# Optimization experiments

Measured on AMD Instinct MI355X. Metric: run time of the kernel, lower is better.

Reference implementation:

```python
import jax, jax.numpy as jnp
import numpy as np

B, N, H, L, K = 8, 2048, 256, 4, 16
G, M0, M1, C = 512, 256, 128, 128
EPS = 1e-5


def _rn(k, shape, scale):
    return jax.random.normal(k, shape, jnp.float32) * jnp.float32(scale)


def setup_inputs() -> dict:
    key = jax.random.key(0)
    ks = jax.random.split(key, 16)
    z, o = jnp.zeros, jnp.ones
    return {
        "x": jax.random.normal(ks[0], (B, N, 3), jnp.float32),
        "batch": jnp.repeat(jnp.arange(B, dtype=jnp.int32)[:, None], N, axis=1),
        "Wf": _rn(ks[1], (3, H), 0.5), "bf": z(H),
        "Wnn": _rn(ks[2], (H, H), H ** -0.5), "bnn": z(H),
        "g1": o((L, H)), "b1": z((L, H)),
        "We": _rn(ks[3], (L, 2 * H, H), (2 * H) ** -0.5), "be": z((L, H)),
        "g2": o((L, H)), "b2": z((L, H)),
        "Wl": _rn(ks[4], (L, H, H), H ** -0.5), "bl": z((L, H)),
        "alpha": _rn(ks[5], (L,), 0.1),
        "gg": o(H), "bgb": z(H),
        "Wg": _rn(ks[6], (H, G), H ** -0.5), "bg2": z(G),
        "Wm1": _rn(ks[7], (G, M0), G ** -0.5), "bm1": z(M0),
        "Wm2": _rn(ks[8], (M0, M1), M0 ** -0.5), "bm2": z(M1),
        "Wm3": _rn(ks[9], (M1, C), M1 ** -0.5), "bm3": z(C),
    }


def _bn(x, g, b):
    # BatchNorm1d training-mode math over all nodes (axes B,N), per channel
    m = x.mean(axis=(0, 1))
    v = x.var(axis=(0, 1))
    return (x - m) * jax.lax.rsqrt(v + EPS) * g + b


def _dgcnn(x, We, be):
    # dynamic kNN graph in feature space, per cloud; x: [B,N,H]
    sq = jnp.sum(x * x, axis=-1)                                  # [B,N]
    d = sq[:, :, None] + sq[:, None, :] - 2.0 * jnp.einsum('bnd,bmd->bnm', x, x)
    idx = jax.lax.top_k(-d, K)[1]                                 # [B,N,K] (includes self)
    x_j = jax.vmap(lambda xb, ib: xb[ib])(x, idx)                 # [B,N,K,H]
    x_i = x[:, :, None, :]
    e = jnp.concatenate([jnp.broadcast_to(x_i, x_j.shape), x_j - x_i], axis=-1)
    msg = jnp.einsum('bnkf,fh->bnkh', e, We) + be                 # edge MLP
    return jnp.max(msg, axis=2)                                   # max aggregate


def _forward(x, Wf, bf, Wnn, bnn, g1, b1, We, be, g2, b2, Wl, bl, alpha,
             gg, bgb, Wg, bg2, Wm1, bm1, Wm2, bm2, Wm3, bm3):
    h = x @ Wf + bf                                               # ffm_x (Linear, scale=None)
    for i in range(L):
        t = h @ Wnn + bnn if i == 0 else h                        # nn_x only on first layer
        t = jax.nn.relu(_bn(t, g1[i], b1[i]))
        t = _dgcnn(t, We[i], be[i])
        t = jax.nn.relu(_bn(t, g2[i], b2[i]))
        t = t @ Wl[i] + bl[i]
        h = h + alpha[i] * t                                      # ResidualCoefficient
    t = jax.nn.relu(_bn(h, gg, bgb)) @ Wg + bg2
    p = jnp.max(t, axis=1)                                        # global max pool -> [B,G]
    p = jax.nn.relu(p @ Wm1 + bm1)
    p = jax.nn.relu(p @ Wm2 + bm2)
    return p @ Wm3 + bm3                                          # [B, n_components]


def reference(x, batch, Wf, bf, Wnn, bnn, g1, b1, We, be, g2, b2, Wl, bl, alpha,
              gg, bgb, Wg, bg2, Wm1, bm1, Wm2, bm2, Wm3, bm3):
    # batch ids are implied by the dense [B,N] layout; kept for signature fidelity
    del batch
    return _forward(x, Wf, bf, Wnn, bnn, g1, b1, We, be, g2, b2, Wl, bl, alpha,
                    gg, bgb, Wg, bg2, Wm1, bm1, Wm2, bm2, Wm3, bm3)
```

## Files before the change

### kernel.cpp

```cpp
#include <hip/hip_runtime.h>
#include <cfloat>

#define B_  8
#define N_  2048
#define H_  256
#define L_  4
#define K_  16
#define G_  512
#define M0_ 256
#define M1_ 128
#define C_  128
#define BN_ 16384
#define KP_ 768

typedef unsigned short ushort_t;
typedef __attribute__((ext_vector_type(8))) short short8;
typedef __attribute__((ext_vector_type(4))) float f32x4;

#define OFF_H     ((size_t)0)
#define OFF_APACK ((size_t)16777216)
#define OFF_SQ    ((size_t)67108864)
#define OFF_IDX   ((size_t)67174400)
#define OFF_STATS ((size_t)68222976)
#define OFF_SCSH  ((size_t)68227072)
#define OFF_BCAT  ((size_t)68229120)
#define OFF_P0    ((size_t)68231168)
#define OFF_P1    ((size_t)68247552)
#define OFF_P2    ((size_t)68255744)
#define OFF_D     ((size_t)69206016)
#define OFF_T     (OFF_D + (size_t)0)
#define OFF_UV    (OFF_D + (size_t)50331648)
#define OFF_QW    (OFF_D + (size_t)83886080)
#define OFF_PMAX  (OFF_D + (size_t)84672512)
#define WS_NEEDED ((size_t)203423744)

static __device__ __forceinline__ ushort_t f2bf(float f) {
    unsigned u = __float_as_uint(f);
    unsigned r = (u + 0x7fffu + ((u >> 16) & 1u)) >> 16;
    return (ushort_t)r;
}
static __device__ __forceinline__ float bf2f(ushort_t h) {
    return __uint_as_float(((unsigned)h) << 16);
}
static __device__ __forceinline__ void pack3(float v, ushort_t* A, size_t base, int f) {
    ushort_t hi = f2bf(v);
    ushort_t lo = f2bf(v - bf2f(hi));
    A[base + f] = hi; A[base + H_ + f] = lo; A[base + 2 * H_ + f] = hi;
}


__global__ void feat_pack(const float* __restrict__ x, const float* __restrict__ Wf,
                          const float* __restrict__ bfv, float* __restrict__ h,
                          ushort_t* __restrict__ Ap) {
    int pt = blockIdx.x;
    int f  = threadIdx.x;
    float x0 = x[pt * 3 + 0], x1 = x[pt * 3 + 1], x2 = x[pt * 3 + 2];
    float v = x0 * Wf[f] + x1 * Wf[H_ + f] + x2 * Wf[2 * H_ + f] + bfv[f];
    h[(size_t)pt * H_ + f] = v;
    pack3(v, Ap, (size_t)pt * KP_, f);
}

__global__ void pack_wT(const float* __restrict__ W, ushort_t* __restrict__ Qp, int Nd) {
    int n = blockIdx.x, k = threadIdx.x;
    float w = W[(size_t)k * Nd + n];
    ushort_t hi = f2bf(w), lo = f2bf(w - bf2f(hi));
    size_t base = (size_t)n * KP_;
    Qp[base + k] = hi; Qp[base + H_ + k] = hi; Qp[base + 2 * H_ + k] = lo;
}

__global__ void pack_qcat(const float* __restrict__ We_l, const float* __restrict__ be_l,
                          ushort_t* __restrict__ Qp, float* __restrict__ bcat) {
    int n = blockIdx.x, k = threadIdx.x;
    float w;
    if (n < H_) w = We_l[(size_t)k * H_ + n] - We_l[(size_t)H_ * H_ + (size_t)k * H_ + n];
    else        w = We_l[(size_t)H_ * H_ + (size_t)k * H_ + (n - H_)];
    ushort_t hi = f2bf(w), lo = f2bf(w - bf2f(hi));
    size_t base = (size_t)n * KP_;
    Qp[base + k] = hi; Qp[base + H_ + k] = hi; Qp[base + 2 * H_ + k] = lo;
    if (k == 0) bcat[n] = (n < H_) ? be_l[n] : 0.f;
}

__global__ __launch_bounds__(256) void mfma_gemm(
    const ushort_t* __restrict__ P, const ushort_t* __restrict__ Q,
    const float* __restrict__ aux, float* __restrict__ out,
    int Kd, int ldOut, int mode, const float* __restrict__ resid,
    const float* __restrict__ alphap, int aidx, double* __restrict__ stats,
    int nx) {
    __shared__ __align__(16) ushort_t As[128 * 32];
    __shared__ __align__(16) ushort_t Bs[128 * 32];
    __shared__ float cs1[4][64], cs2[4][64];
    int i0, j0;
    if (nx) {
        int blk = blockIdx.x;
        int z = blk & 7;
        int rest = blk >> 3;
        int xb = rest % nx;
        int ys = rest / nx;
        i0 = (z * 16 + ys) * 128;
        j0 = xb * 128;
    } else {
        i0 = blockIdx.y * 128; j0 = blockIdx.x * 128;
    }
    int tid = threadIdx.x;
    int lane = tid & 63, wave = tid >> 6;
    int wm = wave & 1, wn = wave >> 1;
    int m16 = lane & 15, kq = (lane >> 4) * 8;

    f32x4 acc[4][4];
    f32x4 zero = {0.f, 0.f, 0.f, 0.f};
#pragma unroll
    for (int i = 0; i < 4; ++i)
#pragma unroll
        for (int j = 0; j < 4; ++j) acc[i][j] = zero;

    int srow = tid >> 2;
    int skc  = (tid & 3) * 8;

    for (int k0 = 0; k0 < Kd; k0 += 32) {
#pragma unroll
        for (int s = 0; s < 2; ++s) {
            int row = srow + s * 64;
            const ushort_t* gpA = P + (size_t)(i0 + row) * Kd + k0 + skc;
            const ushort_t* gpB = Q + (size_t)(j0 + row) * Kd + k0 + skc;
            __builtin_amdgcn_global_load_lds(
                (const __attribute__((address_space(1))) void*)gpA,
                (__attribute__((address_space(3))) void*)(As + (size_t)(wave * 64 + s * 256) * 8),
                16, 0, 0);
            __builtin_amdgcn_global_load_lds(
                (const __attribute__((address_space(1))) void*)gpB,
                (__attribute__((address_space(3))) void*)(Bs + (size_t)(wave * 64 + s * 256) * 8),
                16, 0, 0);
        }
        __syncthreads();
        short8 af[4], bfr[4];
#pragma unroll
        for (int fi = 0; fi < 4; ++fi)
            af[fi] = *(const short8*)(As + (wm * 64 + fi * 16 + m16) * 32 + kq);
#pragma unroll
        for (int fj = 0; fj < 4; ++fj)
            bfr[fj] = *(const short8*)(Bs + (wn * 64 + fj * 16 + m16) * 32 + kq);
#pragma unroll
        for (int fi = 0; fi < 4; ++fi)
#pragma unroll
            for (int fj = 0; fj < 4; ++fj)
                acc[fi][fj] = __builtin_amdgcn_mfma_f32_16x16x32_bf16(
                    af[fi], bfr[fj], acc[fi][fj], 0, 0, 0);
        __syncthreads();
    }
    float alpha = (mode == 2) ? alphap[aidx] : 0.f;
    int rbase = i0 + wm * 64 + (lane >> 4) * 4;
    int cbase = j0 + wn * 64 + m16;
    float s1[4] = {0.f, 0.f, 0.f, 0.f}, s2[4] = {0.f, 0.f, 0.f, 0.f};
#pragma unroll
    for (int fi = 0; fi < 4; ++fi) {
#pragma unroll
        for (int fj = 0; fj < 4; ++fj) {
            int c = cbase + fj * 16;
            float a = aux[c];
#pragma unroll
            for (int r = 0; r < 4; ++r) {
                int gr = rbase + fi * 16 + r;
                size_t oidx = (size_t)gr * ldOut + c;
                float val;
                if (mode == 2) val = resid[oidx] + alpha * (acc[fi][fj][r] + a);
                else           val = acc[fi][fj][r] + a;
                out[oidx] = val;
                s1[fj] += val; s2[fj] += val * val;
            }
        }
    }
    if (stats) {
#pragma unroll
        for (int fj = 0; fj < 4; ++fj) {
            float a1 = s1[fj], a2 = s2[fj];
            a1 += __shfl_xor(a1, 16); a1 += __shfl_xor(a1, 32);
            a2 += __shfl_xor(a2, 16); a2 += __shfl_xor(a2, 32);
            if ((lane >> 4) == 0) {
                cs1[wave][fj * 16 + m16] = a1;
                cs2[wave][fj * 16 + m16] = a2;
            }
        }
        __syncthreads();
        if (tid < 128) {
            int wnl = tid >> 6, cl = tid & 63;
            float t1 = cs1[2 * wnl][cl] + cs1[2 * wnl + 1][cl];
            float t2 = cs2[2 * wnl][cl] + cs2[2 * wnl + 1][cl];
            int c = j0 + tid;
            atomicAdd(&stats[c], (double)t1);
            atomicAdd(&stats[H_ + c], (double)t2);
        }
    }
}

__global__ __launch_bounds__(256) void gram_sym(const ushort_t* __restrict__ Ap,
                                                const float* __restrict__ sqb,
                                                float* __restrict__ D) {
    __shared__ __align__(16) ushort_t As[128 * 32];
    __shared__ __align__(16) ushort_t Bs[128 * 32];
    __shared__ __align__(16) float stg[4][1280];
    int blk = blockIdx.x;
    int z = blk & 7;
    int p = blk >> 3;
    int bi = 0, rem = p;
    while (rem >= 16 - bi) { rem -= 16 - bi; ++bi; }
    int bj = bi + rem;
    const ushort_t* Pz = Ap + (size_t)z * N_ * KP_;
    const float* sqz = sqb + (size_t)z * N_;
    float* Dz = D + (size_t)z * N_ * N_;
    int i0 = bi * 128, j0 = bj * 128;

    int tid = threadIdx.x;
    int lane = tid & 63, wave = tid >> 6;
    int wm = wave & 1, wn = wave >> 1;
    int m16 = lane & 15, q4 = lane >> 4;
    int kq = q4 * 8;

    f32x4 acc[4][4];
    f32x4 zero = {0.f, 0.f, 0.f, 0.f};
#pragma unroll
    for (int i = 0; i < 4; ++i)
#pragma unroll
        for (int j = 0; j < 4; ++j) acc[i][j] = zero;

    int srow = tid >> 2;
    int skc  = (tid & 3) * 8;

    for (int k0 = 0; k0 < KP_; k0 += 32) {
        int kb = (k0 < 256) ? k0 : ((k0 < 512) ? k0 + 256 : k0 - 256);
#pragma unroll
        for (int s = 0; s < 2; ++s) {
            int row = srow + s * 64;
            const ushort_t* gpA = Pz + (size_t)(i0 + row) * KP_ + k0 + skc;
            const ushort_t* gpB = Pz + (size_t)(j0 + row) * KP_ + kb + skc;
            __builtin_amdgcn_global_load_lds(
                (const __attribute__((address_space(1))) void*)gpA,
                (__attribute__((address_space(3))) void*)(As + (size_t)(wave * 64 + s * 256) * 8),
                16, 0, 0);
            __builtin_amdgcn_global_load_lds(
                (const __attribute__((address_space(1))) void*)gpB,
                (__attribute__((address_space(3))) void*)(Bs + (size_t)(wave * 64 + s * 256) * 8),
                16, 0, 0);
        }
        __syncthreads();
        short8 af[4], bfr[4];
#pragma unroll
        for (int fi = 0; fi < 4; ++fi)
            af[fi] = *(const short8*)(As + (wm * 64 + fi * 16 + m16) * 32 + kq);
#pragma unroll
        for (int fj = 0; fj < 4; ++fj)
            bfr[fj] = *(const short8*)(Bs + (wn * 64 + fj * 16 + m16) * 32 + kq);
#pragma unroll
        for (int fi = 0; fi < 4; ++fi)
#pragma unroll
            for (int fj = 0; fj < 4; ++fj)
                acc[fi][fj] = __builtin_amdgcn_mfma_f32_16x16x32_bf16(
                    af[fi], bfr[fj], acc[fi][fj], 0, 0, 0);
        __syncthreads();
    }

    float* sg = stg[wave];
    float scl[4];
#pragma unroll
    for (int fj = 0; fj < 4; ++fj) scl[fj] = sqz[j0 + wn * 64 + fj * 16 + m16];
    float sr[4][4];
#pragma unroll
    for (int fi = 0; fi < 4; ++fi) {
        float4 s4 = *(const float4*)(sqz + i0 + wm * 64 + fi * 16 + q4 * 4);
        sr[fi][0] = s4.x; sr[fi][1] = s4.y; sr[fi][2] = s4.z; sr[fi][3] = s4.w;
    }

    int rr = lane >> 2, cc = lane & 3;
#pragma unroll
    for (int fi = 0; fi < 4; ++fi) {
#pragma unroll
        for (int fj = 0; fj < 4; ++fj)
#pragma unroll
            for (int r = 0; r < 4; ++r)
                sg[(q4 * 4 + r) * 68 + fj * 16 + m16] = scl[fj] - 2.f * acc[fi][fj][r];
        float* drow = Dz + (size_t)(i0 + wm * 64 + fi * 16 + rr) * N_ + j0 + wn * 64;
#pragma unroll
        for (int t = 0; t < 4; ++t) {
            int chunk = cc + 4 * t;
            f32x4 o = *(const f32x4*)(sg + rr * 68 + chunk * 4);
            __builtin_nontemporal_store(o, (f32x4*)(drow + chunk * 4));
        }
    }

    if (bi != bj) {
#pragma unroll
        for (int fi = 0; fi < 4; ++fi) {
#pragma unroll
            for (int fj = 0; fj < 4; ++fj)
#pragma unroll
                for (int r = 0; r < 4; ++r)
                    sg[(fj * 16 + m16) * 20 + q4 * 4 + r] =
                        sr[fi][r] - 2.f * acc[fi][fj][r];
            int chunk = lane & 3;
#pragma unroll
            for (int u = 0; u < 4; ++u) {
                int cr = (lane >> 2) + 16 * u;
                f32x4 o = *(const f32x4*)(sg + cr * 20 + chunk * 4);
                __builtin_nontemporal_store(o,
                    (f32x4*)(Dz + (size_t)(j0 + wn * 64 + cr) * N_ +
                             i0 + wm * 64 + fi * 16 + chunk * 4));
            }
        }
    }
}

__global__ __launch_bounds__(256) void topk16(const float* __restrict__ D,
                                              int* __restrict__ idxb) {
    __shared__ unsigned long long cand[4][256];
    __shared__ int cnt[4];
    int w = threadIdx.x >> 6, lane = threadIdx.x & 63;
    int row = blockIdx.x * 4 + w;
    const float* dp = D + (size_t)row * N_;
    unsigned sk[32];
#pragma unroll
    for (int t = 0; t < 8; ++t) {
        f32x4 v4 = __builtin_nontemporal_load((const f32x4*)(dp + t * 256 + lane * 4));
#pragma unroll
        for (int j = 0; j < 4; ++j) {
            unsigned u = __float_as_uint(v4[j]);
            sk[t * 4 + j] = (u & 0x80000000u) ? ~u : (u | 0x80000000u);
        }
    }
    if (lane == 0) cnt[w] = 0;
    unsigned vm = sk[0];
#pragma unroll
    for (int i = 1; i < 32; ++i) vm = min(vm, sk[i]);
#pragma unroll
    for (int k = 2; k <= 64; k <<= 1) {
#pragma unroll
        for (int j = k >> 1; j > 0; j >>= 1) {
            unsigned pv = __shfl_xor(vm, j);
            bool up = ((lane & k) == 0);
            bool lower = ((lane & j) == 0);
            unsigned mn = min(vm, pv), mx = max(vm, pv);
            vm = (lower == up) ? mn : mx;
        }
    }
    unsigned T = __shfl(vm, 15);
    __syncthreads();
#pragma unroll
    for (int i = 0; i < 32; ++i) {
        if (sk[i] <= T) {
            unsigned col = (unsigned)((i >> 2) * 256 + lane * 4 + (i & 3));
            int s = atomicAdd(&cnt[w], 1);
            if (s < 256) cand[w][s] = ((unsigned long long)sk[i] << 32) | col;
        }
    }
    __syncthreads();
    int cn = cnt[w];
    if (cn <= 64) {
        unsigned long long mykey = (lane < cn) ? cand[w][lane] : ~0ull;
        for (int it = 0; it < 16; ++it) {
            unsigned long long best = mykey;
#pragma unroll
            for (int off = 32; off; off >>= 1) {
                unsigned long long o = __shfl_xor(best, off);
                if (o < best) best = o;
            }
            if (mykey == best) mykey = ~0ull;
            if (lane == 0) idxb[row * 16 + it] = (int)(unsigned)(best & 0xffffffffu);
        }
    } else if (cn <= 256) {
        for (int it = 0; it < 16; ++it) {
            unsigned long long best = ~0ull;
            for (int i = lane; i < cn; i += 64) {
                unsigned long long c = cand[w][i];
                if (c < best) best = c;
            }
#pragma unroll
            for (int off = 32; off; off >>= 1) {
                unsigned long long o = __shfl_xor(best, off);
                if (o < best) best = o;
            }
            for (int i = lane; i < cn; i += 64)
                if (cand[w][i] == best) cand[w][i] = ~0ull;
            if (lane == 0) idxb[row * 16 + it] = (int)(unsigned)(best & 0xffffffffu);
        }
    } else {
        unsigned mask = 0;
        for (int it = 0; it < 16; ++it) {
            unsigned long long key = ~0ull;
#pragma unroll
            for (int i = 0; i < 32; ++i) {
                if (!((mask >> i) & 1u)) {
                    unsigned long long k2 = ((unsigned long long)sk[i] << 32) |
                        (unsigned)((i >> 2) * 256 + lane * 4 + (i & 3));
                    if (k2 < key) key = k2;
                }
            }
#pragma unroll
            for (int off = 32; off; off >>= 1) {
                unsigned long long o = __shfl_xor(key, off);
                if (o < key) key = o;
            }
            unsigned jc = (unsigned)(key & 0xffffffffu);
            int li = ((jc & 255) >> 2);
            int ii = ((jc >> 8) << 2) | (jc & 3);
            if (lane == li) mask |= 1u << ii;
            if (lane == 0) idxb[row * 16 + it] = (int)jc;
        }
    }
}

__global__ void gather_max(const float* __restrict__ uv, const int* __restrict__ idxb,
                           float* __restrict__ outp, double* __restrict__ stats) {
    int blk = blockIdx.x;
    int b = blk & 7;
    int strip = blk >> 3;
    int r0 = b * N_ + strip * 32;
    int f = threadIdx.x;
    float s1 = 0.f, s2 = 0.f;
    for (int rr = 0; rr < 32; ++rr) {
        int row = r0 + rr;
        const int* ip = idxb + row * 16;
        float m = -FLT_MAX;
#pragma unroll
        for (int k = 0; k < 16; ++k) {
            int j = ip[k];
            m = fmaxf(m, uv[((size_t)((b << 11) + j)) * 512 + 256 + f]);
        }
        float v = uv[(size_t)row * 512 + f] + m;
        outp[(size_t)row * H_ + f] = v;
        s1 += v; s2 += v * v;
    }
    atomicAdd(&stats[f], (double)s1);
    atomicAdd(&stats[H_ + f], (double)s2);
}

__global__ void bn_zero(double* s) { s[threadIdx.x] = 0.0; }

__global__ void bn_final(double* __restrict__ sums, const float* __restrict__ g,
                         const float* __restrict__ b, float* __restrict__ scsh) {
    int f = threadIdx.x;
    double m  = sums[f] / (double)BN_;
    double var = sums[H_ + f] / (double)BN_ - m * m;
    double inv = 1.0 / sqrt(var + 1e-5);
    float sc = g[f] * (float)inv;
    scsh[f] = sc;
    scsh[H_ + f] = b[f] - (float)m * sc;
    sums[f] = 0.0; sums[H_ + f] = 0.0;
}

__global__ void bn_apply_pack(const float* __restrict__ X, const float* __restrict__ scsh,
                              ushort_t* __restrict__ Ap, float* __restrict__ sq) {
    int tid = threadIdx.x;
    int row = blockIdx.x * 8 + (tid >> 5);
    int f0  = (tid & 31) * 8;
    const float* xp = X + (size_t)row * H_ + f0;
    f32x4 x0 = *(const f32x4*)(xp);
    f32x4 x1 = *(const f32x4*)(xp + 4);
    f32x4 sc0 = *(const f32x4*)(scsh + f0);
    f32x4 sc1 = *(const f32x4*)(scsh + f0 + 4);
    f32x4 sh0 = *(const f32x4*)(scsh + H_ + f0);
    f32x4 sh1 = *(const f32x4*)(scsh + H_ + f0 + 4);
    float v[8];
#pragma unroll
    for (int i = 0; i < 4; ++i) {
        v[i]     = fmaxf(x0[i] * sc0[i] + sh0[i], 0.f);
        v[i + 4] = fmaxf(x1[i] * sc1[i] + sh1[i], 0.f);
    }
    short8 hi8, lo8;
#pragma unroll
    for (int i = 0; i < 8; ++i) {
        ushort_t hi = f2bf(v[i]);
        ushort_t lo = f2bf(v[i] - bf2f(hi));
        hi8[i] = (short)hi; lo8[i] = (short)lo;
    }
    ushort_t* ap = Ap + (size_t)row * KP_ + f0;
    *(short8*)(ap)            = hi8;
    *(short8*)(ap + H_)       = lo8;
    *(short8*)(ap + 2 * H_)   = hi8;
    if (sq) {
        float s = 0.f;
#pragma unroll
        for (int i = 0; i < 8; ++i) s += v[i] * v[i];
#pragma unroll
        for (int off = 16; off; off >>= 1) s += __shfl_down(s, off, 32);
        if ((tid & 31) == 0) sq[row] = s;
    }
}

__global__ void maxpool1(const float* __restrict__ y, float* __restrict__ pmax) {
    int b = blockIdx.x, gc = blockIdx.y, nc = blockIdx.z;
    int g = gc * 256 + threadIdx.x;
    const float* yb = y + ((size_t)b * N_ + (size_t)nc * 128) * G_;
    float m = -FLT_MAX;
    for (int n = 0; n < 128; ++n) m = fmaxf(m, yb[(size_t)n * G_ + g]);
    pmax[((size_t)(b * 16 + nc)) * G_ + g] = m;
}

__global__ void maxpool2(const float* __restrict__ pmax, float* __restrict__ p) {
    int b = blockIdx.x;
    int g = blockIdx.y * 256 + threadIdx.x;
    float m = -FLT_MAX;
    for (int c = 0; c < 16; ++c) m = fmaxf(m, pmax[((size_t)(b * 16 + c)) * G_ + g]);
    p[(size_t)b * G_ + g] = m;
}

__global__ __launch_bounds__(256) void head_gemm(const float* __restrict__ A,
                                                 const float* __restrict__ W,
                                                 const float* __restrict__ bias,
                                                 float* __restrict__ Cc,
                                                 int Kd, int Nd, int relu) {
    int m = blockIdx.x;
    int c0 = blockIdx.y * 64;
    int cl = threadIdx.x & 63;
    int ks = threadIdx.x >> 6;
    int kper = Kd >> 2;
    const float* Ap = A + (size_t)m * Kd + (size_t)ks * kper;
    const float* Wp = W + (size_t)ks * kper * Nd + c0 + cl;
    float acc = 0.f;
    for (int k = 0; k < kper; k += 8) {
#pragma unroll
        for (int u2 = 0; u2 < 8; ++u2)
            acc += Ap[k + u2] * Wp[(size_t)(k + u2) * Nd];
    }
    __shared__ float red[4][64];
    red[ks][cl] = acc;
    __syncthreads();
    if (ks == 0) {
        float s = red[0][cl] + red[1][cl] + red[2][cl] + red[3][cl] + bias[c0 + cl];
        if (relu) s = fmaxf(s, 0.f);
        Cc[(size_t)m * Nd + c0 + cl] = s;
    }
}

extern "C" void kernel_launch(void* const* d_in, const int* in_sizes, int n_in,
                              void* d_out, int out_size, void* d_ws, size_t ws_size,
                              hipStream_t stream) {
    (void)in_sizes; (void)n_in; (void)out_size;
    if (ws_size < WS_NEEDED) return;

    const float* x    = (const float*)d_in[0];
    const float* Wf   = (const float*)d_in[2];
    const float* bfv  = (const float*)d_in[3];
    const float* Wnn  = (const float*)d_in[4];
    const float* bnn  = (const float*)d_in[5];
    const float* g1   = (const float*)d_in[6];
    const float* b1   = (const float*)d_in[7];
    const float* We   = (const float*)d_in[8];
    const float* be   = (const float*)d_in[9];
    const float* g2   = (const float*)d_in[10];
    const float* b2   = (const float*)d_in[11];
    const float* Wl   = (const float*)d_in[12];
    const float* bl   = (const float*)d_in[13];
    const float* alpha= (const float*)d_in[14];
    const float* gg   = (const float*)d_in[15];
    const float* bgb  = (const float*)d_in[16];
    const float* Wg   = (const float*)d_in[17];
    const float* bg2  = (const float*)d_in[18];
    const float* Wm1  = (const float*)d_in[19];
    const float* bm1  = (const float*)d_in[20];
    const float* Wm2  = (const float*)d_in[21];
    const float* bm2  = (const float*)d_in[22];
    const float* Wm3  = (const float*)d_in[23];
    const float* bm3  = (const float*)d_in[24];
    float* outp = (float*)d_out;

    char* ws = (char*)d_ws;
    float*    h    = (float*)(ws + OFF_H);
    ushort_t* Ap   = (ushort_t*)(ws + OFF_APACK);
    float*    sqb  = (float*)(ws + OFF_SQ);
    int*      idxb = (int*)  (ws + OFF_IDX);
    double*   stats= (double*)(ws + OFF_STATS);
    float*    scsh = (float*)(ws + OFF_SCSH);
    float*    bcat = (float*)(ws + OFF_BCAT);
    float*    p0   = (float*)(ws + OFF_P0);
    float*    p1   = (float*)(ws + OFF_P1);
    float*    p2   = (float*)(ws + OFF_P2);
    float*    dmat = (float*)(ws + OFF_D);
    float*    t    = (float*)(ws + OFF_T);
    float*    uv   = (float*)(ws + OFF_UV);
    float*    y    = (float*)(ws + OFF_UV);
    ushort_t* Qw   = (ushort_t*)(ws + OFF_QW);
    float*    pmax = (float*)(ws + OFF_PMAX);

    hipLaunchKernelGGL(bn_zero, dim3(1), dim3(512), 0, stream, stats);

    hipLaunchKernelGGL(feat_pack, dim3(BN_), dim3(256), 0, stream, x, Wf, bfv, h, Ap);
    hipLaunchKernelGGL(pack_wT, dim3(H_), dim3(256), 0, stream, Wnn, Qw, H_);
    hipLaunchKernelGGL(mfma_gemm, dim3(256), dim3(256), 0, stream,
                       Ap, Qw, bnn, t, KP_, H_, 0,
                       (const float*)nullptr, (const float*)nullptr, 0, stats, 2);

    for (int l = 0; l < L_; ++l) {
        const float* src1 = (l == 0) ? t : h;
        hipLaunchKernelGGL(bn_final, dim3(1), dim3(256), 0, stream,
                           stats, g1 + l * H_, b1 + l * H_, scsh);
        hipLaunchKernelGGL(bn_apply_pack, dim3(BN_ / 8), dim3(256), 0, stream,
                           src1, scsh, Ap, sqb);
        hipLaunchKernelGGL(gram_sym, dim3(1088), dim3(256), 0, stream,
                           Ap, sqb, dmat);
        hipLaunchKernelGGL(topk16, dim3(BN_ / 4), dim3(256), 0, stream, dmat, idxb);
        hipLaunchKernelGGL(pack_qcat, dim3(512), dim3(256), 0, stream,
                           We + (size_t)l * 2 * H_ * H_, be + (size_t)l * H_, Qw, bcat);
        hipLaunchKernelGGL(mfma_gemm, dim3(512), dim3(256), 0, stream,
                           Ap, Qw, bcat, uv, KP_, 512, 0,
                           (const float*)nullptr, (const float*)nullptr, 0,
                           (double*)nullptr, 4);
        hipLaunchKernelGGL(gather_max, dim3(512), dim3(256), 0, stream,
                           uv, idxb, t, stats);
        hipLaunchKernelGGL(bn_final, dim3(1), dim3(256), 0, stream,
                           stats, g2 + l * H_, b2 + l * H_, scsh);
        hipLaunchKernelGGL(bn_apply_pack, dim3(BN_ / 8), dim3(256), 0, stream,
                           t, scsh, Ap, (float*)nullptr);
        hipLaunchKernelGGL(pack_wT, dim3(H_), dim3(256), 0, stream,
                           Wl + (size_t)l * H_ * H_, Qw, H_);
        hipLaunchKernelGGL(mfma_gemm, dim3(256), dim3(256), 0, stream,
                           Ap, Qw, bl + (size_t)l * H_, h, KP_, H_, 2,
                           h, alpha, l, stats, 2);
    }

    hipLaunchKernelGGL(bn_final, dim3(1), dim3(256), 0, stream, stats, gg, bgb, scsh);
    hipLaunchKernelGGL(bn_apply_pack, dim3(BN_ / 8), dim3(256), 0, stream,
                       h, scsh, Ap, (float*)nullptr);
    hipLaunchKernelGGL(pack_wT, dim3(G_), dim3(256), 0, stream, Wg, Qw, G_);
    hipLaunchKernelGGL(mfma_gemm, dim3(512), dim3(256), 0, stream,
                       Ap, Qw, bg2, y, KP_, G_, 0,
                       (const float*)nullptr, (const float*)nullptr, 0,
                       (double*)nullptr, 4);
    hipLaunchKernelGGL(maxpool1, dim3(8, 2, 16), dim3(256), 0, stream, y, pmax);
    hipLaunchKernelGGL(maxpool2, dim3(8, 2), dim3(256), 0, stream, pmax, p0);
    hipLaunchKernelGGL(head_gemm, dim3(8, 4), dim3(256), 0, stream, p0, Wm1, bm1, p1, G_, M0_, 1);
    hipLaunchKernelGGL(head_gemm, dim3(8, 2), dim3(256), 0, stream, p1, Wm2, bm2, p2, M0_, M1_, 1);
    hipLaunchKernelGGL(head_gemm, dim3(8, 2), dim3(256), 0, stream, p2, Wm3, bm3, outp, M1_, C_, 0);
}
```

Baseline: 1.132 ms.

## Emit per-32-column chunk minima from gram kernel to prune top-k reads

The Gram-distance kernel now also computes, for each row, the minimum distance within every 32-column chunk and writes these 64 minima per row to a new workspace buffer. The top-k kernel uses these chunk minima to find a threshold at the 16th smallest, then loads only the chunks whose minimum is at or below it instead of reading the full 2048-wide row. This cuts global read traffic in top-k. In exchange gram_sym does extra shuffles and scattered stores, and the full-row fallback path still exists for rows with many candidates.

Measured after the change: 1.266 ms. 1.12x slower.

```diff
diff --git a/kernel.cpp b/kernel.cpp
--- a/kernel.cpp
+++ b/kernel.cpp
@@ -19,6 +19,7 @@
 
 #define OFF_H     ((size_t)0)
 #define OFF_APACK ((size_t)16777216)
+#define OFF_CMIN  ((size_t)41943040)
 #define OFF_SQ    ((size_t)67108864)
 #define OFF_IDX   ((size_t)67174400)
 #define OFF_STATS ((size_t)68222976)
@@ -46,6 +47,10 @@
     ushort_t hi = f2bf(v);
     ushort_t lo = f2bf(v - bf2f(hi));
     A[base + f] = hi; A[base + H_ + f] = lo; A[base + 2 * H_ + f] = hi;
+}
+static __device__ __forceinline__ unsigned sortkey(float v) {
+    unsigned u = __float_as_uint(v);
+    return (u & 0x80000000u) ? ~u : (u | 0x80000000u);
 }
 
 
@@ -194,7 +199,8 @@
 
 __global__ __launch_bounds__(256) void gram_sym(const ushort_t* __restrict__ Ap,
                                                 const float* __restrict__ sqb,
-                                                float* __restrict__ D) {
+                                                float* __restrict__ D,
+                                                float* __restrict__ cminb) {
     __shared__ __align__(16) ushort_t As[128 * 32];
     __shared__ __align__(16) ushort_t Bs[128 * 32];
     __shared__ __align__(16) float stg[4][1280];
@@ -207,6 +213,7 @@
     const ushort_t* Pz = Ap + (size_t)z * N_ * KP_;
     const float* sqz = sqb + (size_t)z * N_;
     float* Dz = D + (size_t)z * N_ * N_;
+    float* cz = cminb + (size_t)z * N_ * 64;
     int i0 = bi * 128, j0 = bj * 128;
 
     int tid = threadIdx.x;
@@ -269,6 +276,45 @@
         sr[fi][0] = s4.x; sr[fi][1] = s4.y; sr[fi][2] = s4.z; sr[fi][3] = s4.w;
     }
 
+#pragma unroll
+    for (int fi = 0; fi < 4; ++fi) {
+#pragma unroll
+        for (int r = 0; r < 4; ++r) {
+            float m0 = fminf(scl[0] - 2.f * acc[fi][0][r], scl[1] - 2.f * acc[fi][1][r]);
+            float m1 = fminf(scl[2] - 2.f * acc[fi][2][r], scl[3] - 2.f * acc[fi][3][r]);
+#pragma unroll
+            for (int off = 1; off < 16; off <<= 1) {
+                m0 = fminf(m0, __shfl_xor(m0, off));
+                m1 = fminf(m1, __shfl_xor(m1, off));
+            }
+            if (m16 == 0) {
+                int row = i0 + wm * 64 + fi * 16 + q4 * 4 + r;
+                cz[(size_t)row * 64 + bj * 4 + wn * 2 + 0] = m0;
+                cz[(size_t)row * 64 + bj * 4 + wn * 2 + 1] = m1;
+            }
+        }
+    }
+    if (bi != bj) {
+#pragma unroll
+        for (int fj = 0; fj < 4; ++fj) {
+            float mp0 = FLT_MAX, mp1 = FLT_MAX;
+#pragma unroll
+            for (int r = 0; r < 4; ++r) {
+                mp0 = fminf(mp0, fminf(sr[0][r] - 2.f * acc[0][fj][r],
+                                       sr[1][r] - 2.f * acc[1][fj][r]));
+                mp1 = fminf(mp1, fminf(sr[2][r] - 2.f * acc[2][fj][r],
+                                       sr[3][r] - 2.f * acc[3][fj][r]));
+            }
+            mp0 = fminf(mp0, __shfl_xor(mp0, 16)); mp0 = fminf(mp0, __shfl_xor(mp0, 32));
+            mp1 = fminf(mp1, __shfl_xor(mp1, 16)); mp1 = fminf(mp1, __shfl_xor(mp1, 32));
+            if (q4 == 0) {
+                int row = j0 + wn * 64 + fj * 16 + m16;
+                cz[(size_t)row * 64 + bi * 4 + wm * 2 + 0] = mp0;
+                cz[(size_t)row * 64 + bi * 4 + wm * 2 + 1] = mp1;
+            }
+        }
+    }
+
     int rr = lane >> 2, cc = lane & 3;
 #pragma unroll
     for (int fi = 0; fi < 4; ++fi) {
@@ -309,26 +355,17 @@
 }
 
 __global__ __launch_bounds__(256) void topk16(const float* __restrict__ D,
+                                              const float* __restrict__ cminb,
                                               int* __restrict__ idxb) {
     __shared__ unsigned long long cand[4][256];
     __shared__ int cnt[4];
     int w = threadIdx.x >> 6, lane = threadIdx.x & 63;
     int row = blockIdx.x * 4 + w;
     const float* dp = D + (size_t)row * N_;
-    unsigned sk[32];
-#pragma unroll
-    for (int t = 0; t < 8; ++t) {
-        f32x4 v4 = __builtin_nontemporal_load((const f32x4*)(dp + t * 256 + lane * 4));
-#pragma unroll
-        for (int j = 0; j < 4; ++j) {
-            unsigned u = __float_as_uint(v4[j]);
-            sk[t * 4 + j] = (u & 0x80000000u) ? ~u : (u | 0x80000000u);
-        }
-    }
+    float cm = cminb[(size_t)row * 64 + lane];
+    unsigned mykey = sortkey(cm);
     if (lane == 0) cnt[w] = 0;
-    unsigned vm = sk[0];
-#pragma unroll
-    for (int i = 1; i < 32; ++i) vm = min(vm, sk[i]);
+    unsigned vm = mykey;
 #pragma unroll
     for (int k = 2; k <= 64; k <<= 1) {
 #pragma unroll
@@ -341,27 +378,38 @@
         }
     }
     unsigned T = __shfl(vm, 15);
+    unsigned long long act = __ballot(mykey <= T);
     __syncthreads();
-#pragma unroll
-    for (int i = 0; i < 32; ++i) {
-        if (sk[i] <= T) {
-            unsigned col = (unsigned)((i >> 2) * 256 + lane * 4 + (i & 3));
-            int s = atomicAdd(&cnt[w], 1);
-            if (s < 256) cand[w][s] = ((unsigned long long)sk[i] << 32) | col;
+    int half = lane >> 5, sub = lane & 31;
+    unsigned long long a = act;
+    while (a) {
+        int c0 = __ffsll((long long)a) - 1; a &= a - 1;
+        int c1 = -1;
+        if (a) { c1 = __ffsll((long long)a) - 1; a &= a - 1; }
+        int c = half ? c1 : c0;
+        if (c >= 0) {
+            int col = c * 32 + sub;
+            float v = __builtin_nontemporal_load(dp + col);
+            unsigned sk2 = sortkey(v);
+            if (sk2 <= T) {
+                int s = atomicAdd(&cnt[w], 1);
+                if (s < 256)
+                    cand[w][s] = ((unsigned long long)sk2 << 32) | (unsigned)col;
+            }
         }
     }
     __syncthreads();
     int cn = cnt[w];
     if (cn <= 64) {
-        unsigned long long mykey = (lane < cn) ? cand[w][lane] : ~0ull;
+        unsigned long long mk = (lane < cn) ? cand[w][lane] : ~0ull;
         for (int it = 0; it < 16; ++it) {
-            unsigned long long best = mykey;
+            unsigned long long best = mk;
 #pragma unroll
             for (int off = 32; off; off >>= 1) {
                 unsigned long long o = __shfl_xor(best, off);
                 if (o < best) best = o;
             }
-            if (mykey == best) mykey = ~0ull;
+            if (mk == best) mk = ~0ull;
             if (lane == 0) idxb[row * 16 + it] = (int)(unsigned)(best & 0xffffffffu);
         }
     } else if (cn <= 256) {
@@ -381,6 +429,13 @@
             if (lane == 0) idxb[row * 16 + it] = (int)(unsigned)(best & 0xffffffffu);
         }
     } else {
+        unsigned sk[32];
+#pragma unroll
+        for (int t = 0; t < 8; ++t) {
+            f32x4 v4 = __builtin_nontemporal_load((const f32x4*)(dp + t * 256 + lane * 4));
+#pragma unroll
+            for (int j = 0; j < 4; ++j) sk[t * 4 + j] = sortkey(v4[j]);
+        }
         unsigned mask = 0;
         for (int it = 0; it < 16; ++it) {
             unsigned long long key = ~0ull;
@@ -564,6 +619,7 @@
     char* ws = (char*)d_ws;
     float*    h    = (float*)(ws + OFF_H);
     ushort_t* Ap   = (ushort_t*)(ws + OFF_APACK);
+    float*    cmin = (float*)(ws + OFF_CMIN);
     float*    sqb  = (float*)(ws + OFF_SQ);
     int*      idxb = (int*)  (ws + OFF_IDX);
     double*   stats= (double*)(ws + OFF_STATS);
@@ -594,8 +650,9 @@
         hipLaunchKernelGGL(bn_apply_pack, dim3(BN_ / 8), dim3(256), 0, stream,
                            src1, scsh, Ap, sqb);
         hipLaunchKernelGGL(gram_sym, dim3(1088), dim3(256), 0, stream,
-                           Ap, sqb, dmat);
-        hipLaunchKernelGGL(topk16, dim3(BN_ / 4), dim3(256), 0, stream, dmat, idxb);
+                           Ap, sqb, dmat, cmin);
+        hipLaunchKernelGGL(topk16, dim3(BN_ / 4), dim3(256), 0, stream,
+                           dmat, cmin, idxb);
         hipLaunchKernelGGL(pack_qcat, dim3(512), dim3(256), 0, stream,
                            We + (size_t)l * 2 * H_ * H_, be + (size_t)l * H_, Qw, bcat);
         hipLaunchKernelGGL(mfma_gemm, dim3(512), dim3(256), 0, stream,
```
